# Performance work log

Measured on AMD Instinct MI355X. Metric: run time of the kernel, lower is better.

## Reference

```python
import jax, jax.numpy as jnp
import numpy as np

EMBED_DIM = 1024
NUM_HEADS = 16
HEAD_DIM = EMBED_DIM // NUM_HEADS
BATCH = 2
SEQ = 2048


def setup_inputs() -> dict:
    key = jax.random.key(0)
    ks = jax.random.split(key, 9)
    s = 1.0 / np.sqrt(EMBED_DIM)
    return {
        "x": jax.random.normal(ks[0], (BATCH, SEQ, EMBED_DIM), jnp.float32),
        "mask": jnp.ones((BATCH, SEQ), jnp.int32),
        "Wq": jax.random.normal(ks[1], (EMBED_DIM, EMBED_DIM), jnp.float32) * s,
        "bq": jax.random.normal(ks[2], (EMBED_DIM,), jnp.float32) * s,
        "Wk": jax.random.normal(ks[3], (EMBED_DIM, EMBED_DIM), jnp.float32) * s,
        "bk": jax.random.normal(ks[4], (EMBED_DIM,), jnp.float32) * s,
        "Wv": jax.random.normal(ks[5], (EMBED_DIM, EMBED_DIM), jnp.float32) * s,
        "bv": jax.random.normal(ks[6], (EMBED_DIM,), jnp.float32) * s,
        "Wo": jax.random.normal(ks[7], (EMBED_DIM, EMBED_DIM), jnp.float32) * s,
        "bo": jax.random.normal(ks[8], (EMBED_DIM,), jnp.float32) * s,
    }


def reference(x, mask, Wq, bq, Wk, bk, Wv, bv, Wo, bo):
    B, S, E = x.shape
    H, D = NUM_HEADS, HEAD_DIM
    # torch Linear: y = x @ W.T + b
    q = (x @ Wq.T + bq).reshape(B, S, H, D).transpose(0, 2, 1, 3)  # [B,H,S,D]
    k = (x @ Wk.T + bk).reshape(B, S, H, D).transpose(0, 2, 1, 3)
    v = (x @ Wv.T + bv).reshape(B, S, H, D).transpose(0, 2, 1, 3)
    scores = jnp.einsum("bhqd,bhkd->bhqk", q, k) / jnp.sqrt(jnp.float32(D))
    # mask: [B,S] -> [B,1,1,S]; fill masked positions with -1e9
    scores = jnp.where(mask[:, None, None, :] == 0, jnp.float32(-1e9), scores)
    probs = jax.nn.softmax(scores, axis=-1)
    # dropout omitted: original stores a float and would crash; eval semantics = identity
    attn = jnp.einsum("bhqk,bhkd->bhqd", probs, v)  # [B,H,S,D]
    attn = attn.transpose(0, 2, 1, 3).reshape(B, S, E)
    return attn @ Wo.T + bo
```

## Files before the change

### kernel.cpp

```cpp
#include <hip/hip_runtime.h>
#include <stdint.h>

#define S_LEN 2048
#define EMB   1024
#define NH    16
#define HD    64
#define BK 64

typedef __bf16 bf16x8 __attribute__((ext_vector_type(8)));
typedef short  short4v __attribute__((ext_vector_type(4)));
typedef unsigned int uint2v __attribute__((ext_vector_type(2)));
typedef float  floatx4 __attribute__((ext_vector_type(4)));

#if defined(__has_builtin)
#if __has_builtin(__builtin_amdgcn_mfma_f32_16x16x16bf16_1k)
#define HAVE_MFMA16 1
#endif
#if __has_builtin(__builtin_amdgcn_exp2f)
#define EXP2F __builtin_amdgcn_exp2f
#endif
#endif
#ifndef EXP2F
#define EXP2F exp2f
#endif

#define QSCALE 0.1803368801111204f

__device__ __forceinline__ unsigned short f2bf(float f) {
  unsigned u = __builtin_bit_cast(unsigned, f);
  u += 0x7fffu + ((u >> 16) & 1u);
  return (unsigned short)(u >> 16);
}
__device__ __forceinline__ unsigned short f2bf_hu(float f) {
  return (unsigned short)((__builtin_bit_cast(unsigned, f) + 0x8000u) >> 16);
}
__device__ __forceinline__ unsigned packbf2(float a, float b) {
  unsigned ua = __builtin_bit_cast(unsigned, a) + 0x8000u;
  unsigned ub = __builtin_bit_cast(unsigned, b) + 0x8000u;
  return __builtin_amdgcn_perm(ub, ua, 0x07060302);
}

__global__ __launch_bounds__(256) void cvt_all(const float* __restrict__ x,
                                               const float* __restrict__ Wq,
                                               const float* __restrict__ Wk,
                                               const float* __restrict__ Wv,
                                               const float* __restrict__ Wo,
                                               unsigned short* __restrict__ xb,
                                               unsigned short* __restrict__ Wqb,
                                               unsigned short* __restrict__ Wkb,
                                               unsigned short* __restrict__ Wvb,
                                               unsigned short* __restrict__ Wob) {
  int blk = blockIdx.x;
  const float* s; unsigned short* d; int off;
  if (blk < 4096)      { s = x;  d = xb;  off = blk; }
  else if (blk < 5120) { s = Wq; d = Wqb; off = blk - 4096; }
  else if (blk < 6144) { s = Wk; d = Wkb; off = blk - 5120; }
  else if (blk < 7168) { s = Wv; d = Wvb; off = blk - 6144; }
  else                 { s = Wo; d = Wob; off = blk - 7168; }
  int i = (off * 256 + threadIdx.x) * 4;
  float4 v = *(const float4*)(s + i);
  ushort4 o;
  o.x = f2bf(v.x); o.y = f2bf(v.y); o.z = f2bf(v.z); o.w = f2bf(v.w);
  *(ushort4*)(d + i) = o;
}

__device__ __forceinline__ void stage16(const void* g, void* l) {
  __builtin_amdgcn_global_load_lds(
      (const __attribute__((address_space(1))) void*)g,
      (__attribute__((address_space(3))) void*)l, 16, 0, 0);
}

__global__ __launch_bounds__(256, 3) void qkv_gemm(const unsigned short* __restrict__ xb,
                                                   const unsigned short* __restrict__ Wqb,
                                                   const unsigned short* __restrict__ Wkb,
                                                   const unsigned short* __restrict__ Wvb,
                                                   const float* __restrict__ bq,
                                                   const float* __restrict__ bk,
                                                   const float* __restrict__ bv,
                                                   unsigned short* __restrict__ Qb,
                                                   unsigned short* __restrict__ Kb,
                                                   unsigned short* __restrict__ Vtb) {
  __shared__ unsigned short As[128 * BK];
  __shared__ unsigned short Bs[128 * BK];
  const int z = blockIdx.z;
  const unsigned short* Bm = (z == 0) ? Wqb : (z == 1) ? Wkb : Wvb;
  const float* bias        = (z == 0) ? bq  : (z == 1) ? bk  : bv;
  unsigned short* outp     = (z == 0) ? Qb  : (z == 1) ? Kb  : Vtb;
  const float scale = (z == 0) ? QSCALE : 1.0f;
  const int mode = (z == 2) ? 2 : 1;

  const int tid  = threadIdx.x;
  const int lane = tid & 63;
  const int wave = tid >> 6;
  const int m16  = lane & 15;
  const int quad = lane >> 4;
  const int m0 = blockIdx.x * 128;
  const int n0 = blockIdx.y * 128;
  const int wrow = (wave >> 1) * 64;
  const int wcol = (wave & 1) * 64;
  const int K = 1024;

  floatx4 acc[4][4];
  for (int i = 0; i < 4; ++i)
    for (int j = 0; j < 4; ++j) acc[i][j] = floatx4{0.f, 0.f, 0.f, 0.f};

  for (int k0 = 0; k0 < K; k0 += BK) {
    __syncthreads();
    for (int i = 0; i < 4; ++i) {
      int c = i * 256 + tid;
      int row = c >> 3, col = (c & 7) << 3;
      stage16(xb + (size_t)(m0 + row) * K + k0 + col,
              (char*)As + (size_t)(i * 256 + wave * 64) * 16);
      stage16(Bm + (size_t)(n0 + row) * K + k0 + col,
              (char*)Bs + (size_t)(i * 256 + wave * 64) * 16);
    }
    __syncthreads();
    for (int kk = 0; kk < 2; ++kk) {
      bf16x8 af[4], bfr[4];
      for (int ti = 0; ti < 4; ++ti)
        af[ti] = *(const bf16x8*)(As + (wrow + ti * 16 + m16) * BK + kk * 32 + quad * 8);
      for (int tj = 0; tj < 4; ++tj)
        bfr[tj] = *(const bf16x8*)(Bs + (wcol + tj * 16 + m16) * BK + kk * 32 + quad * 8);
      for (int ti = 0; ti < 4; ++ti)
        for (int tj = 0; tj < 4; ++tj)
          acc[ti][tj] = __builtin_amdgcn_mfma_f32_16x16x32_bf16(bfr[tj], af[ti], acc[ti][tj], 0, 0, 0);
    }
  }

  if (mode == 1) {
    for (int ti = 0; ti < 4; ++ti) {
      int m = m0 + wrow + ti * 16 + m16;
      int b = m >> 11, ss = m & 2047;
      for (int tj = 0; tj < 4; ++tj) {
        int n = n0 + wcol + tj * 16 + quad * 4;
        int hh = n >> 6, d = n & 63;
        float4 b4 = *(const float4*)(bias + n);
        float v0 = (acc[ti][tj][0] + b4.x) * scale;
        float v1 = (acc[ti][tj][1] + b4.y) * scale;
        float v2 = (acc[ti][tj][2] + b4.z) * scale;
        float v3 = (acc[ti][tj][3] + b4.w) * scale;
        uint2v pk{packbf2(v0, v1), packbf2(v2, v3)};
        *(uint2v*)((unsigned short*)outp +
                   ((size_t)(b * NH + hh) * S_LEN + ss) * HD + d) = pk;
      }
    }
  } else {
    for (int tj = 0; tj < 4; ++tj)
      for (int reg = 0; reg < 4; ++reg) {
        int n = n0 + wcol + tj * 16 + quad * 4 + reg;
        int hh = n >> 6, d = n & 63;
        float bv = bias[n];
        for (int ti = 0; ti < 4; ++ti) {
          int m = m0 + wrow + ti * 16 + m16;
          int b = m >> 11, ss = m & 2047;
          ((unsigned short*)outp)[((size_t)(b * NH + hh) * HD + d) * S_LEN + ss] =
              f2bf_hu(acc[ti][tj][reg] + bv);
        }
      }
  }
}

__global__ __launch_bounds__(256, 4) void out_gemm(const unsigned short* __restrict__ Ab,
                                                   const unsigned short* __restrict__ Wob,
                                                   const float* __restrict__ bo,
                                                   float* __restrict__ out) {
  __shared__ unsigned short As[128 * BK];
  __shared__ unsigned short Bs[64 * BK];
  const int tid  = threadIdx.x;
  const int lane = tid & 63;
  const int wave = tid >> 6;
  const int m16  = lane & 15;
  const int quad = lane >> 4;
  const int m0 = blockIdx.x * 128;
  const int n0 = blockIdx.y * 64;
  const int wrow = (wave >> 1) * 64;
  const int wcol = (wave & 1) * 32;
  const int K = 1024, N = 1024;

  floatx4 acc[4][2];
  for (int i = 0; i < 4; ++i)
    for (int j = 0; j < 2; ++j) acc[i][j] = floatx4{0.f, 0.f, 0.f, 0.f};

  for (int k0 = 0; k0 < K; k0 += BK) {
    __syncthreads();
    for (int i = 0; i < 4; ++i) {
      int c = i * 256 + tid;
      int row = c >> 3, col = (c & 7) << 3;
      stage16(Ab + (size_t)(m0 + row) * K + k0 + col,
              (char*)As + (size_t)(i * 256 + wave * 64) * 16);
    }
    for (int i = 0; i < 2; ++i) {
      int c = i * 256 + tid;
      int row = c >> 3, col = (c & 7) << 3;
      stage16(Wob + (size_t)(n0 + row) * K + k0 + col,
              (char*)Bs + (size_t)(i * 256 + wave * 64) * 16);
    }
    __syncthreads();
    for (int kk = 0; kk < 2; ++kk) {
      bf16x8 af[4], bfr[2];
      for (int ti = 0; ti < 4; ++ti)
        af[ti] = *(const bf16x8*)(As + (wrow + ti * 16 + m16) * BK + kk * 32 + quad * 8);
      for (int tj = 0; tj < 2; ++tj)
        bfr[tj] = *(const bf16x8*)(Bs + (wcol + tj * 16 + m16) * BK + kk * 32 + quad * 8);
      for (int ti = 0; ti < 4; ++ti)
        for (int tj = 0; tj < 2; ++tj)
          acc[ti][tj] = __builtin_amdgcn_mfma_f32_16x16x32_bf16(af[ti], bfr[tj], acc[ti][tj], 0, 0, 0);
    }
  }

  for (int tj = 0; tj < 2; ++tj) {
    int n = n0 + wcol + tj * 16 + m16;
    float bv = bo[n];
    for (int ti = 0; ti < 4; ++ti)
      for (int reg = 0; reg < 4; ++reg) {
        int m = m0 + wrow + ti * 16 + quad * 4 + reg;
        out[(size_t)m * N + n] = acc[ti][tj][reg] + bv;
      }
  }
}

__global__ __launch_bounds__(256, 4) void attn_kernel(const unsigned short* __restrict__ Qb,
                                                      const unsigned short* __restrict__ Kb,
                                                      const unsigned short* __restrict__ Vtb,
                                                      const int* __restrict__ mask,
                                                      unsigned short* __restrict__ attnb) {
  __shared__ unsigned short Ks[2 * 64 * 64];
  __shared__ unsigned short Vts[2 * 64 * 64];
  __shared__ int zw[4];
#ifndef HAVE_MFMA16
  __shared__ unsigned short Pq[4 * 16 * 72];
#endif

  const int tid  = threadIdx.x;
  const int lane = tid & 63;
  const int wave = tid >> 6;
  const int m16  = lane & 15;
  const int quad = lane >> 4;
  const int bh = blockIdx.x;
  const int qt = blockIdx.y;
  const int b  = bh >> 4;
  const int h  = bh & 15;
  const int q0 = qt * 128;
  const size_t head = (size_t)bh * S_LEN * HD;

  bf16x8 qf[2][2];
  for (int qs = 0; qs < 2; ++qs) {
    const unsigned short* qrow = Qb + head + (size_t)(q0 + wave * 32 + qs * 16 + m16) * HD;
    qf[qs][0] = *(const bf16x8*)(qrow + quad * 8);
    qf[qs][1] = *(const bf16x8*)(qrow + 32 + quad * 8);
  }

  const int kr = lane >> 3, kc = lane & 7;
  const unsigned short* kg0 = Kb + head + (size_t)(wave * 16 + kr) * HD + ((kc ^ kr) << 3);
  const unsigned short* vg0 = Vtb + head + (size_t)(wave * 16 + kr) * S_LEN + ((kc ^ kr) << 3);
  const int* mrow = mask + b * S_LEN;

#define STAGE_KV(pp, kb_)                                                      \
  {                                                                            \
    const unsigned short* ksrc = kg0 + (size_t)(kb_) * 64 * HD;                \
    char* kdst = (char*)Ks + (pp) * 8192 + wave * 2048;                        \
    stage16(ksrc,           kdst);                                             \
    stage16(ksrc + 8 * HD,  kdst + 1024);                                      \
    const unsigned short* vsrc = vg0 + (kb_) * 64;                             \
    char* vdst = (char*)Vts + (pp) * 8192 + wave * 2048;                       \
    stage16(vsrc,              vdst);                                          \
    stage16(vsrc + 8 * S_LEN,  vdst + 1024);                                   \
  }

  float l_run[2] = {0.f, 0.f};
  floatx4 acc_o[2][4];
  for (int qs = 0; qs < 2; ++qs)
    for (int ti = 0; ti < 4; ++ti) acc_o[qs][ti] = floatx4{0.f, 0.f, 0.f, 0.f};

  {
    const int4* mp = (const int4*)(mrow + tid * 8);
    int4 a = mp[0], c4 = mp[1];
    bool z = (a.x & a.y & a.z & a.w & c4.x & c4.y & c4.z & c4.w) == 0;
    unsigned long long bal = __ballot(z);
    if (lane == 0) zw[wave] = (bal != 0ull) ? 1 : 0;
  }

  STAGE_KV(0, 0);
  __syncthreads();
  const bool anymask = (zw[0] | zw[1] | zw[2] | zw[3]) != 0;

  const int xs = m16 & 7;
  const floatx4 fz = floatx4{0.f, 0.f, 0.f, 0.f};

  for (int kb = 0; kb < 32; ++kb) {
    const int p = kb & 1;
    const unsigned short* Kp = Ks + p * 4096;
    const unsigned short* Vp = Vts + p * 4096;
    if (kb < 31) STAGE_KV(p ^ 1, kb + 1);

    floatx4 acc_s[2][4];
    {
      bf16x8 kf[4];
      for (int tj = 0; tj < 4; ++tj)
        kf[tj] = *(const bf16x8*)&Kp[(tj * 16 + m16) * 64 + ((quad ^ xs) << 3)];
      for (int tj = 0; tj < 4; ++tj) {
        acc_s[0][tj] = __builtin_amdgcn_mfma_f32_16x16x32_bf16(kf[tj], qf[0][0], fz, 0, 0, 0);
        acc_s[1][tj] = __builtin_amdgcn_mfma_f32_16x16x32_bf16(kf[tj], qf[1][0], fz, 0, 0, 0);
      }
      for (int tj = 0; tj < 4; ++tj)
        kf[tj] = *(const bf16x8*)&Kp[(tj * 16 + m16) * 64 + (((4 + quad) ^ xs) << 3)];
      for (int tj = 0; tj < 4; ++tj) {
        acc_s[0][tj] = __builtin_amdgcn_mfma_f32_16x16x32_bf16(kf[tj], qf[0][1], acc_s[0][tj], 0, 0, 0);
        acc_s[1][tj] = __builtin_amdgcn_mfma_f32_16x16x32_bf16(kf[tj], qf[1][1], acc_s[1][tj], 0, 0, 0);
      }
    }

    unsigned up[2][8];
    for (int qs = 0; qs < 2; ++qs) {
      if (anymask) {
        for (int t = 0; t < 4; ++t)
          for (int r = 0; r < 4; ++r) {
            int idx = kb * 64 + t * 16 + quad * 4 + r;
            acc_s[qs][t][r] += (mrow[idx] == 0) ? -1e9f : 0.f;
          }
      }
      float sl = 0.f;
      for (int i = 0; i < 8; ++i) {
        float p0 = EXP2F(acc_s[qs][i >> 1][(i & 1) * 2]);
        float p1 = EXP2F(acc_s[qs][i >> 1][(i & 1) * 2 + 1]);
        sl += p0 + p1;
        up[qs][i] = packbf2(p0, p1);
      }
      l_run[qs] += sl;
    }

#ifdef HAVE_MFMA16
    for (int ti = 0; ti < 4; ++ti)
      for (int c = 0; c < 4; ++c) {
        short4v vf = *(const short4v*)&Vp[(ti * 16 + m16) * 64 +
                                          (((2 * c + (quad >> 1)) ^ xs) << 3) +
                                          ((quad & 1) << 2)];
        short4v Pb0 = __builtin_bit_cast(short4v, uint2v{up[0][2 * c], up[0][2 * c + 1]});
        short4v Pb1 = __builtin_bit_cast(short4v, uint2v{up[1][2 * c], up[1][2 * c + 1]});
        acc_o[0][ti] = __builtin_amdgcn_mfma_f32_16x16x16bf16_1k(vf, Pb0, acc_o[0][ti], 0, 0, 0);
        acc_o[1][ti] = __builtin_amdgcn_mfma_f32_16x16x16bf16_1k(vf, Pb1, acc_o[1][ti], 0, 0, 0);
      }
#else
    {
      unsigned short* Pw = Pq + wave * 16 * 72;
      for (int qs = 0; qs < 2; ++qs) {
        for (int t = 0; t < 4; ++t) {
          *(unsigned*)&Pw[m16 * 72 + t * 16 + quad * 4]     = up[qs][2 * t];
          *(unsigned*)&Pw[m16 * 72 + t * 16 + quad * 4 + 2] = up[qs][2 * t + 1];
        }
        for (int kk = 0; kk < 2; ++kk) {
          bf16x8 pf = *(const bf16x8*)&Pw[m16 * 72 + kk * 32 + quad * 8];
          for (int ti = 0; ti < 4; ++ti) {
            bf16x8 vfb = *(const bf16x8*)&Vp[(ti * 16 + m16) * 64 +
                                             (((kk * 4 + quad) ^ xs) << 3)];
            acc_o[qs][ti] = __builtin_amdgcn_mfma_f32_16x16x32_bf16(vfb, pf, acc_o[qs][ti], 0, 0, 0);
          }
        }
      }
    }
#endif

    __syncthreads();
  }

  for (int qs = 0; qs < 2; ++qs) {
    l_run[qs] += __shfl_xor(l_run[qs], 16);
    l_run[qs] += __shfl_xor(l_run[qs], 32);
    float rl = 1.f / l_run[qs];
    int orow = q0 + wave * 32 + qs * 16 + m16;
    for (int ti = 0; ti < 4; ++ti) {
      ushort4 o;
      o.x = f2bf_hu(acc_o[qs][ti][0] * rl);
      o.y = f2bf_hu(acc_o[qs][ti][1] * rl);
      o.z = f2bf_hu(acc_o[qs][ti][2] * rl);
      o.w = f2bf_hu(acc_o[qs][ti][3] * rl);
      int e = h * HD + ti * 16 + quad * 4;
      *(ushort4*)&attnb[((size_t)(b * S_LEN + orow)) * EMB + e] = o;
    }
  }
#undef STAGE_KV
}

extern "C" void kernel_launch(void* const* d_in, const int* in_sizes, int n_in,
                              void* d_out, int out_size, void* d_ws, size_t ws_size,
                              hipStream_t stream) {
  const float* x  = (const float*)d_in[0];
  const int* mask = (const int*)d_in[1];
  const float* Wq = (const float*)d_in[2];
  const float* bq = (const float*)d_in[3];
  const float* Wk = (const float*)d_in[4];
  const float* bk = (const float*)d_in[5];
  const float* Wv = (const float*)d_in[6];
  const float* bv = (const float*)d_in[7];
  const float* Wo = (const float*)d_in[8];
  const float* bo = (const float*)d_in[9];
  float* out = (float*)d_out;

  char* ws = (char*)d_ws;
  unsigned short* xb  = (unsigned short*)(ws);
  unsigned short* Wqb = (unsigned short*)(ws + 8388608);
  unsigned short* Wkb = (unsigned short*)(ws + 10485760);
  unsigned short* Wvb = (unsigned short*)(ws + 12582912);
  unsigned short* Wob = (unsigned short*)(ws + 14680064);
  unsigned short* Qb  = (unsigned short*)(ws + 16777216);
  unsigned short* Kbb = (unsigned short*)(ws + 25165824);
  unsigned short* Vtb = (unsigned short*)(ws + 33554432);
  unsigned short* Ab  = (unsigned short*)(ws + 41943040);

  cvt_all<<<dim3(8192), dim3(256), 0, stream>>>(x, Wq, Wk, Wv, Wo, xb, Wqb, Wkb, Wvb, Wob);
  qkv_gemm<<<dim3(32, 8, 3), dim3(256), 0, stream>>>(xb, Wqb, Wkb, Wvb, bq, bk, bv, Qb, Kbb, Vtb);
  attn_kernel<<<dim3(32, 16), dim3(256), 0, stream>>>(Qb, Kbb, Vtb, mask, Ab);
  out_gemm<<<dim3(32, 16), dim3(256), 0, stream>>>(Ab, Wob, bo, out);
}
```

Baseline: 199.0 us.

## Split attention KV range in two and merge partials in output GEMM

The attention kernel now splits the 2048-key range into two halves along a new grid dimension, doubling block count from 512 to 1024. Each half writes unnormalized fp16 partial outputs and row sums. The output GEMM combines the two partials, normalizes and converts to bf16 while staging its A tile. This raises occupancy on the attention stage but adds extra global traffic for the fp16 partials, and moves A staging from async copies to register loads. The merge relies on the max-free exp2 softmax, so partials can be summed directly; fp16 partials risk overflow.

```diff
diff --git a/kernel.cpp b/kernel.cpp
--- a/kernel.cpp
+++ b/kernel.cpp
@@ -10,7 +10,10 @@
 typedef __bf16 bf16x8 __attribute__((ext_vector_type(8)));
 typedef short  short4v __attribute__((ext_vector_type(4)));
 typedef unsigned int uint2v __attribute__((ext_vector_type(2)));
+typedef unsigned int uint4v __attribute__((ext_vector_type(4)));
 typedef float  floatx4 __attribute__((ext_vector_type(4)));
+typedef _Float16 half4v __attribute__((ext_vector_type(4)));
+typedef _Float16 half8v __attribute__((ext_vector_type(8)));
 
 #if defined(__has_builtin)
 #if __has_builtin(__builtin_amdgcn_mfma_f32_16x16x16bf16_1k)
@@ -160,12 +163,14 @@
   }
 }
 
-__global__ __launch_bounds__(256, 4) void out_gemm(const unsigned short* __restrict__ Ab,
+__global__ __launch_bounds__(256, 4) void out_gemm(const _Float16* __restrict__ Oph,
+                                                   const float* __restrict__ Lp,
                                                    const unsigned short* __restrict__ Wob,
                                                    const float* __restrict__ bo,
                                                    float* __restrict__ out) {
   __shared__ unsigned short As[128 * BK];
   __shared__ unsigned short Bs[64 * BK];
+  __shared__ float rLs[128 * 16];
   const int tid  = threadIdx.x;
   const int lane = tid & 63;
   const int wave = tid >> 6;
@@ -177,23 +182,38 @@
   const int wcol = (wave & 1) * 32;
   const int K = 1024, N = 1024;
 
+  for (int e = 0; e < 8; ++e) {
+    int idx = tid * 8 + e;
+    int m = m0 + (idx >> 4);
+    rLs[idx] = 1.f / (Lp[(size_t)m * 16 + (idx & 15)] +
+                      Lp[(size_t)65536 + (size_t)m * 16 + (idx & 15)]);
+  }
+
   floatx4 acc[4][2];
   for (int i = 0; i < 4; ++i)
     for (int j = 0; j < 2; ++j) acc[i][j] = floatx4{0.f, 0.f, 0.f, 0.f};
 
   for (int k0 = 0; k0 < K; k0 += BK) {
     __syncthreads();
-    for (int i = 0; i < 4; ++i) {
-      int c = i * 256 + tid;
-      int row = c >> 3, col = (c & 7) << 3;
-      stage16(Ab + (size_t)(m0 + row) * K + k0 + col,
-              (char*)As + (size_t)(i * 256 + wave * 64) * 16);
-    }
+    const int hh = k0 >> 6;
     for (int i = 0; i < 2; ++i) {
       int c = i * 256 + tid;
       int row = c >> 3, col = (c & 7) << 3;
       stage16(Wob + (size_t)(n0 + row) * K + k0 + col,
               (char*)Bs + (size_t)(i * 256 + wave * 64) * 16);
+    }
+    for (int i = 0; i < 4; ++i) {
+      int c = i * 256 + tid;
+      int row = c >> 3, col = (c & 7) << 3;
+      int m = m0 + row;
+      half8v x1 = *(const half8v*)(Oph + (size_t)m * EMB + k0 + col);
+      half8v x2 = *(const half8v*)(Oph + (size_t)(4096 + m) * EMB + k0 + col);
+      float r = rLs[row * 16 + hh];
+      unsigned u0 = packbf2(((float)x1[0] + (float)x2[0]) * r, ((float)x1[1] + (float)x2[1]) * r);
+      unsigned u1 = packbf2(((float)x1[2] + (float)x2[2]) * r, ((float)x1[3] + (float)x2[3]) * r);
+      unsigned u2 = packbf2(((float)x1[4] + (float)x2[4]) * r, ((float)x1[5] + (float)x2[5]) * r);
+      unsigned u3 = packbf2(((float)x1[6] + (float)x2[6]) * r, ((float)x1[7] + (float)x2[7]) * r);
+      *(uint4v*)((char*)As + (size_t)c * 16) = uint4v{u0, u1, u2, u3};
     }
     __syncthreads();
     for (int kk = 0; kk < 2; ++kk) {
@@ -223,7 +243,8 @@
                                                       const unsigned short* __restrict__ Kb,
                                                       const unsigned short* __restrict__ Vtb,
                                                       const int* __restrict__ mask,
-                                                      unsigned short* __restrict__ attnb) {
+                                                      _Float16* __restrict__ Oph,
+                                                      float* __restrict__ Lp) {
   __shared__ unsigned short Ks[2 * 64 * 64];
   __shared__ unsigned short Vts[2 * 64 * 64];
   __shared__ int zw[4];
@@ -238,10 +259,12 @@
   const int quad = lane >> 4;
   const int bh = blockIdx.x;
   const int qt = blockIdx.y;
+  const int split = blockIdx.z;
   const int b  = bh >> 4;
-  const int h  = bh & 15;
+  const int hh = bh & 15;
   const int q0 = qt * 128;
   const size_t head = (size_t)bh * S_LEN * HD;
+  const int kvbase = split * 1024;
 
   bf16x8 qf[2][2];
   for (int qs = 0; qs < 2; ++qs) {
@@ -251,8 +274,8 @@
   }
 
   const int kr = lane >> 3, kc = lane & 7;
-  const unsigned short* kg0 = Kb + head + (size_t)(wave * 16 + kr) * HD + ((kc ^ kr) << 3);
-  const unsigned short* vg0 = Vtb + head + (size_t)(wave * 16 + kr) * S_LEN + ((kc ^ kr) << 3);
+  const unsigned short* kg0 = Kb + head + (size_t)(kvbase + wave * 16 + kr) * HD + ((kc ^ kr) << 3);
+  const unsigned short* vg0 = Vtb + head + (size_t)(wave * 16 + kr) * S_LEN + kvbase + ((kc ^ kr) << 3);
   const int* mrow = mask + b * S_LEN;
 
 #define STAGE_KV(pp, kb_)                                                      \
@@ -273,9 +296,8 @@
     for (int ti = 0; ti < 4; ++ti) acc_o[qs][ti] = floatx4{0.f, 0.f, 0.f, 0.f};
 
   {
-    const int4* mp = (const int4*)(mrow + tid * 8);
-    int4 a = mp[0], c4 = mp[1];
-    bool z = (a.x & a.y & a.z & a.w & c4.x & c4.y & c4.z & c4.w) == 0;
+    int4 a = *(const int4*)(mrow + kvbase + tid * 4);
+    bool z = (a.x & a.y & a.z & a.w) == 0;
     unsigned long long bal = __ballot(z);
     if (lane == 0) zw[wave] = (bal != 0ull) ? 1 : 0;
   }
@@ -287,11 +309,11 @@
   const int xs = m16 & 7;
   const floatx4 fz = floatx4{0.f, 0.f, 0.f, 0.f};
 
-  for (int kb = 0; kb < 32; ++kb) {
+  for (int kb = 0; kb < 16; ++kb) {
     const int p = kb & 1;
     const unsigned short* Kp = Ks + p * 4096;
     const unsigned short* Vp = Vts + p * 4096;
-    if (kb < 31) STAGE_KV(p ^ 1, kb + 1);
+    if (kb < 15) STAGE_KV(p ^ 1, kb + 1);
 
     floatx4 acc_s[2][4];
     {
@@ -315,7 +337,7 @@
       if (anymask) {
         for (int t = 0; t < 4; ++t)
           for (int r = 0; r < 4; ++r) {
-            int idx = kb * 64 + t * 16 + quad * 4 + r;
+            int idx = kvbase + kb * 64 + t * 16 + quad * 4 + r;
             acc_s[qs][t][r] += (mrow[idx] == 0) ? -1e9f : 0.f;
           }
       }
@@ -366,16 +388,17 @@
   for (int qs = 0; qs < 2; ++qs) {
     l_run[qs] += __shfl_xor(l_run[qs], 16);
     l_run[qs] += __shfl_xor(l_run[qs], 32);
-    float rl = 1.f / l_run[qs];
     int orow = q0 + wave * 32 + qs * 16 + m16;
+    size_t mrow_g = (size_t)(split * 4096 + b * 2048 + orow);
+    if (quad == 0) Lp[mrow_g * 16 + hh] = l_run[qs];
     for (int ti = 0; ti < 4; ++ti) {
-      ushort4 o;
-      o.x = f2bf_hu(acc_o[qs][ti][0] * rl);
-      o.y = f2bf_hu(acc_o[qs][ti][1] * rl);
-      o.z = f2bf_hu(acc_o[qs][ti][2] * rl);
-      o.w = f2bf_hu(acc_o[qs][ti][3] * rl);
-      int e = h * HD + ti * 16 + quad * 4;
-      *(ushort4*)&attnb[((size_t)(b * S_LEN + orow)) * EMB + e] = o;
+      half4v ho;
+      ho[0] = (_Float16)acc_o[qs][ti][0];
+      ho[1] = (_Float16)acc_o[qs][ti][1];
+      ho[2] = (_Float16)acc_o[qs][ti][2];
+      ho[3] = (_Float16)acc_o[qs][ti][3];
+      int e = hh * HD + ti * 16 + quad * 4;
+      *(half4v*)&Oph[mrow_g * EMB + e] = ho;
     }
   }
 #undef STAGE_KV
@@ -405,10 +428,11 @@
   unsigned short* Qb  = (unsigned short*)(ws + 16777216);
   unsigned short* Kbb = (unsigned short*)(ws + 25165824);
   unsigned short* Vtb = (unsigned short*)(ws + 33554432);
-  unsigned short* Ab  = (unsigned short*)(ws + 41943040);
+  _Float16* Oph       = (_Float16*)(ws + 41943040);
+  float* Lp           = (float*)(ws + 58720256);
 
   cvt_all<<<dim3(8192), dim3(256), 0, stream>>>(x, Wq, Wk, Wv, Wo, xb, Wqb, Wkb, Wvb, Wob);
   qkv_gemm<<<dim3(32, 8, 3), dim3(256), 0, stream>>>(xb, Wqb, Wkb, Wvb, bq, bk, bv, Qb, Kbb, Vtb);
-  attn_kernel<<<dim3(32, 16), dim3(256), 0, stream>>>(Qb, Kbb, Vtb, mask, Ab);
-  out_gemm<<<dim3(32, 16), dim3(256), 0, stream>>>(Ab, Wob, bo, out);
-}
+  attn_kernel<<<dim3(32, 16, 2), dim3(256), 0, stream>>>(Qb, Kbb, Vtb, mask, Oph, Lp);
+  out_gemm<<<dim3(32, 16), dim3(256), 0, stream>>>(Oph, Lp, Wob, bo, out);
+}
```

Result: slower. 215.4 us (+8.2%).
